# Performance work log

Measured on AMD Instinct MI355X. Metric: run time of the kernel, lower is better.

Reference implementation:

```python
import jax, jax.numpy as jnp
import numpy as np

N = 100000      # nodes
E = 1600000     # edges (avg degree 16)
IN, H, H4, OUT = 2, 128, 32, 64
B = 1000        # batch_size for final view


def setup_inputs() -> dict:
    key = jax.random.key(0)
    ks = jax.random.split(key, 16)
    w = lambda k, s: (jax.random.normal(k, s, jnp.float32) * (1.0 / np.sqrt(s[0])))
    return {
        "x": jax.random.normal(ks[0], (N, IN), jnp.float32),
        "edge_index": jax.random.randint(ks[1], (2, E), 0, N, dtype=jnp.int32),
        "batch_size": B,
        "W1": w(ks[2], (IN, H)),  "b1": jnp.zeros((H,), jnp.float32),
        "W2": w(ks[3], (H, H)),   "b2": jnp.zeros((H,), jnp.float32),
        "W3": w(ks[4], (H, H4)),  "b3": jnp.zeros((H4,), jnp.float32),
        "W4": w(ks[5], (H4, H4)), "b4": jnp.zeros((H4,), jnp.float32),
        "W5": w(ks[6], (H4, OUT)),"b5": jnp.zeros((OUT,), jnp.float32),
        "Wl": w(ks[7], (OUT, 1)), "bl": jnp.zeros((1,), jnp.float32),
    }


def gcn_conv(x, src, dst, W, b, n):
    # PyG GCNConv: add self-loops, symmetric degree normalization, scatter-add.
    h = x @ W  # [N, F]
    deg = jax.ops.segment_sum(jnp.ones(src.shape[0], h.dtype), dst,
                              num_segments=n) + 1.0  # +1 for self-loop
    dinv = jax.lax.rsqrt(deg)  # deg >= 1, no inf
    norm = dinv[src] * dinv[dst]  # [E]
    agg = jax.ops.segment_sum(h[src] * norm[:, None], dst, num_segments=n)
    agg = agg + h * (dinv * dinv)[:, None]  # self-loop contribution
    return agg + b


def reference(x, edge_index, batch_size, W1, b1, W2, b2, W3, b3, W4, b4, W5, b5, Wl, bl):
    x = x.reshape(-1, 2)
    n = x.shape[0]
    src, dst = edge_index[0], edge_index[1]
    for W, b in ((W1, b1), (W2, b2), (W3, b3), (W4, b4), (W5, b5)):
        x = jax.nn.relu(gcn_conv(x, src, dst, W, b, n))
    x = x @ Wl + bl  # [N, 1]
    return x.reshape(batch_size, -1)
```

## Files before the change

kernel.cpp:

```cpp
#include <hip/hip_runtime.h>
#include <math.h>


static inline int cdiv(int a, int b) { return (a + b - 1) / b; }

__global__ void zero_i32(int* __restrict__ p, int n) {
    int i = blockIdx.x * 256 + threadIdx.x;
    if (i < n) p[i] = 0;
}

__global__ void count_q(const int* __restrict__ src, const int* __restrict__ dst,
                        int* __restrict__ cntq, int E, int q1) {
    int e = blockIdx.x * 256 + threadIdx.x;
    if (e < E) {
        int s = src[e];
        int q = (s >= q1) + (s >= 2 * q1) + (s >= 3 * q1);
        atomicAdd(&cntq[dst[e] * 4 + q], 1);
    }
}

__global__ void scan1q(const int* __restrict__ cntq, int* __restrict__ off,
                       int* __restrict__ bsum, int n) {
    __shared__ int sm[256];
    int i = blockIdx.x * 256 + threadIdx.x;
    int v = 0;
    if (i < n) {
        int4 c = *reinterpret_cast<const int4*>(cntq + 4 * (size_t)i);
        v = c.x + c.y + c.z + c.w;
    }
    sm[threadIdx.x] = v;
    __syncthreads();
    for (int ofs = 1; ofs < 256; ofs <<= 1) {
        int t = (threadIdx.x >= (unsigned)ofs) ? sm[threadIdx.x - ofs] : 0;
        __syncthreads();
        sm[threadIdx.x] += t;
        __syncthreads();
    }
    if (i < n) off[i] = sm[threadIdx.x];
    if (threadIdx.x == 255) bsum[blockIdx.x] = sm[255];
}

__global__ void scan2(const int* __restrict__ bsum, int* __restrict__ bpre,
                      int nb, int* __restrict__ off, int N, int E) {
    __shared__ int sm[512];
    int t = threadIdx.x;
    sm[t] = (t < nb) ? bsum[t] : 0;
    __syncthreads();
    for (int ofs = 1; ofs < 512; ofs <<= 1) {
        int v = (t >= ofs) ? sm[t - ofs] : 0;
        __syncthreads();
        sm[t] += v;
        __syncthreads();
    }
    if (t < nb) bpre[t] = sm[t] - bsum[t];
    if (t == 0) off[N] = E;
}

__global__ void scan3_fused(const int* __restrict__ cntq, const int* __restrict__ bpre,
                            int* __restrict__ off, int* __restrict__ cursorq,
                            const float* __restrict__ x, float* __restrict__ dinv,
                            float* __restrict__ xs, int n) {
    int i = blockIdx.x * 256 + threadIdx.x;
    if (i < n) {
        int4 cq = *reinterpret_cast<const int4*>(cntq + 4 * (size_t)i);
        int c = cq.x + cq.y + cq.z + cq.w;
        int o = off[i] - c + bpre[blockIdx.x];
        off[i] = o;
        int4 cur;
        cur.x = o;
        cur.y = o + cq.x;
        cur.z = o + cq.x + cq.y;
        cur.w = o + cq.x + cq.y + cq.z;
        *reinterpret_cast<int4*>(cursorq + 4 * (size_t)i) = cur;
        float dv = 1.0f / sqrtf((float)c + 1.0f);
        dinv[i] = dv;
        float2 xv = *reinterpret_cast<const float2*>(x + 2 * (size_t)i);
        *reinterpret_cast<float2*>(xs + 2 * (size_t)i) = float2{dv * xv.x, dv * xv.y};
    }
}

__global__ __launch_bounds__(256) void fill_ranged(const int* __restrict__ src,
                                                   const int* __restrict__ dst,
                                                   int* __restrict__ cursorq,
                                                   int* __restrict__ csr,
                                                   int E, int N, int echunk, int q1) {
    int cls = blockIdx.x & 7;
    int chunk = blockIdx.x >> 3;
    int per = (N + 7) >> 3;
    int lo = cls * per;
    int hi = lo + per; if (hi > N) hi = N;
    int e0 = chunk * echunk;
    int e1 = e0 + echunk; if (e1 > E) e1 = E;
    for (int e = e0 + (int)threadIdx.x; e < e1; e += 256) {
        int d = dst[e];
        if (d >= lo && d < hi) {
            int s = src[e];
            int q = (s >= q1) + (s >= 2 * q1) + (s >= 3 * q1);
            int p = atomicAdd(&cursorq[d * 4 + q], 1);
            csr[p] = s;
        }
    }
}

__global__ __launch_bounds__(256) void agg2_kernel(const float* __restrict__ xs,
                                                   const int* __restrict__ off,
                                                   const int* __restrict__ csr,
                                                   const float* __restrict__ dinv,
                                                   float* __restrict__ out, int n) {
    int v = blockIdx.x * 256 + threadIdx.x;
    if (v >= n) return;
    float a0 = 0.f, a1 = 0.f;
    int e0 = off[v], e1 = off[v + 1];
    for (int e = e0; e < e1; e++) {
        int s = csr[e];
        float2 q = *reinterpret_cast<const float2*>(xs + 2 * (size_t)s);
        a0 += q.x;
        a1 += q.y;
    }
    float dv = dinv[v];
    float2 xv = *reinterpret_cast<const float2*>(xs + 2 * (size_t)v);
    *reinterpret_cast<float2*>(out + 2 * (size_t)v) =
        float2{dv * (a0 + xv.x), dv * (a1 + xv.y)};
}

template <bool BR, bool PS>
__global__ __launch_bounds__(256) void agg128x_kernel(const float* __restrict__ hc,
                                                      const int* __restrict__ off,
                                                      const int* __restrict__ csr,
                                                      const float* __restrict__ dinv,
                                                      const float* __restrict__ bias,
                                                      float* __restrict__ outc, int n) {
    int cls = blockIdx.x & 7;
    int chunk = cls >> 1;
    int half = cls & 1;
    int n2 = (n + 1) >> 1;
    int lo = half * n2;
    int hi = lo + n2; if (hi > n) hi = n;

    const float* __restrict__ h = hc + (size_t)chunk * n * 32;
    float* __restrict__ out = outc + (size_t)chunk * n * 32;

    int tid = threadIdx.x;
    int lane = tid & 63;
    int sl = lane & 7;
    int subbase = lane & ~7;
    int wave = tid >> 6;
    int v = lo + (blockIdx.x >> 3) * 32 + wave * 8 + (lane >> 3);
    if (v >= hi) return;

    int start = off[v];
    int end = off[v + 1];

    float4 acc = {0.f, 0.f, 0.f, 0.f};

    for (int base = start; base < end; base += 16) {
        int m = end - base;
        if (m > 16) m = 16;
        int idxA = (sl < m) ? csr[base + sl] : 0;
        int idxB = (8 + sl < m) ? csr[base + 8 + sl] : 0;
        if (m == 16) {
            float4 hb[16];
#pragma unroll
            for (int u = 0; u < 16; u++) {
                int s = __shfl((u < 8) ? idxA : idxB, subbase + (u & 7));
                hb[u] = *reinterpret_cast<const float4*>(h + (size_t)s * 32 + sl * 4);
            }
#pragma unroll
            for (int u = 0; u < 16; u++) {
                acc.x += hb[u].x; acc.y += hb[u].y; acc.z += hb[u].z; acc.w += hb[u].w;
            }
        } else {
            int ma = (m < 8) ? m : 8;
            int i = 0;
            for (; i + 4 <= ma; i += 4) {
                float4 hb[4];
#pragma unroll
                for (int u = 0; u < 4; u++) {
                    int s = __shfl(idxA, subbase + i + u);
                    hb[u] = *reinterpret_cast<const float4*>(h + (size_t)s * 32 + sl * 4);
                }
#pragma unroll
                for (int u = 0; u < 4; u++) {
                    acc.x += hb[u].x; acc.y += hb[u].y; acc.z += hb[u].z; acc.w += hb[u].w;
                }
            }
            if (i + 2 <= ma) {
                int s0 = __shfl(idxA, subbase + i);
                int s1 = __shfl(idxA, subbase + i + 1);
                float4 h0 = *reinterpret_cast<const float4*>(h + (size_t)s0 * 32 + sl * 4);
                float4 h1 = *reinterpret_cast<const float4*>(h + (size_t)s1 * 32 + sl * 4);
                acc.x += h0.x + h1.x; acc.y += h0.y + h1.y;
                acc.z += h0.z + h1.z; acc.w += h0.w + h1.w;
                i += 2;
            }
            if (i < ma) {
                int s0 = __shfl(idxA, subbase + i);
                float4 h0 = *reinterpret_cast<const float4*>(h + (size_t)s0 * 32 + sl * 4);
                acc.x += h0.x; acc.y += h0.y; acc.z += h0.z; acc.w += h0.w;
            }
            if (m > 8) {
                int mb = m - 8;
                int j = 0;
                for (; j + 4 <= mb; j += 4) {
                    float4 hb[4];
#pragma unroll
                    for (int u = 0; u < 4; u++) {
                        int s = __shfl(idxB, subbase + j + u);
                        hb[u] = *reinterpret_cast<const float4*>(h + (size_t)s * 32 + sl * 4);
                    }
#pragma unroll
                    for (int u = 0; u < 4; u++) {
                        acc.x += hb[u].x; acc.y += hb[u].y; acc.z += hb[u].z; acc.w += hb[u].w;
                    }
                }
                if (j + 2 <= mb) {
                    int s0 = __shfl(idxB, subbase + j);
                    int s1 = __shfl(idxB, subbase + j + 1);
                    float4 h0 = *reinterpret_cast<const float4*>(h + (size_t)s0 * 32 + sl * 4);
                    float4 h1 = *reinterpret_cast<const float4*>(h + (size_t)s1 * 32 + sl * 4);
                    acc.x += h0.x + h1.x; acc.y += h0.y + h1.y;
                    acc.z += h0.z + h1.z; acc.w += h0.w + h1.w;
                    j += 2;
                }
                if (j < mb) {
                    int s0 = __shfl(idxB, subbase + j);
                    float4 h0 = *reinterpret_cast<const float4*>(h + (size_t)s0 * 32 + sl * 4);
                    acc.x += h0.x; acc.y += h0.y; acc.z += h0.z; acc.w += h0.w;
                }
            }
        }
    }

    float dv = dinv[v];
    float4 hv = *reinterpret_cast<const float4*>(h + (size_t)v * 32 + sl * 4);
    float o0 = dv * (acc.x + hv.x);
    float o1 = dv * (acc.y + hv.y);
    float o2 = dv * (acc.z + hv.z);
    float o3 = dv * (acc.w + hv.w);
    if constexpr (BR) {
        float4 b = *reinterpret_cast<const float4*>(bias + chunk * 32 + sl * 4);
        o0 = fmaxf(o0 + b.x, 0.f);
        o1 = fmaxf(o1 + b.y, 0.f);
        o2 = fmaxf(o2 + b.z, 0.f);
        o3 = fmaxf(o3 + b.w, 0.f);
    }
    if constexpr (PS) {
        o0 *= dv; o1 *= dv; o2 *= dv; o3 *= dv;
    }
    *reinterpret_cast<float4*>(out + (size_t)v * 32 + sl * 4) = float4{o0, o1, o2, o3};
}

template <bool BR, bool PS>
__global__ __launch_bounds__(256) void agg32_kernel(const float* __restrict__ h,
                                                    const int* __restrict__ off,
                                                    const int* __restrict__ csr,
                                                    const float* __restrict__ dinv,
                                                    const float* __restrict__ bias,
                                                    float* __restrict__ out, int n) {
    int tid = threadIdx.x;
    int lane = tid & 63;
    int sl = lane & 7;
    int subbase = lane & ~7;
    int wave = tid >> 6;
    int v = blockIdx.x * 32 + wave * 8 + (lane >> 3);
    if (v >= n) return;

    int start = off[v];
    int end = off[v + 1];

    float4 acc = {0.f, 0.f, 0.f, 0.f};

    for (int base = start; base < end; base += 16) {
        int m = end - base;
        if (m > 16) m = 16;
        int idxA = (sl < m) ? csr[base + sl] : 0;
        int idxB = (8 + sl < m) ? csr[base + 8 + sl] : 0;
        if (m == 16) {
            float4 hb[16];
#pragma unroll
            for (int u = 0; u < 16; u++) {
                int s = __shfl((u < 8) ? idxA : idxB, subbase + (u & 7));
                hb[u] = *reinterpret_cast<const float4*>(h + (size_t)s * 32 + sl * 4);
            }
#pragma unroll
            for (int u = 0; u < 16; u++) {
                acc.x += hb[u].x; acc.y += hb[u].y; acc.z += hb[u].z; acc.w += hb[u].w;
            }
        } else {
            int ma = (m < 8) ? m : 8;
            int i = 0;
            for (; i + 4 <= ma; i += 4) {
                float4 hb[4];
#pragma unroll
                for (int u = 0; u < 4; u++) {
                    int s = __shfl(idxA, subbase + i + u);
                    hb[u] = *reinterpret_cast<const float4*>(h + (size_t)s * 32 + sl * 4);
                }
#pragma unroll
                for (int u = 0; u < 4; u++) {
                    acc.x += hb[u].x; acc.y += hb[u].y; acc.z += hb[u].z; acc.w += hb[u].w;
                }
            }
            if (i + 2 <= ma) {
                int s0 = __shfl(idxA, subbase + i);
                int s1 = __shfl(idxA, subbase + i + 1);
                float4 h0 = *reinterpret_cast<const float4*>(h + (size_t)s0 * 32 + sl * 4);
                float4 h1 = *reinterpret_cast<const float4*>(h + (size_t)s1 * 32 + sl * 4);
                acc.x += h0.x + h1.x; acc.y += h0.y + h1.y;
                acc.z += h0.z + h1.z; acc.w += h0.w + h1.w;
                i += 2;
            }
            if (i < ma) {
                int s0 = __shfl(idxA, subbase + i);
                float4 h0 = *reinterpret_cast<const float4*>(h + (size_t)s0 * 32 + sl * 4);
                acc.x += h0.x; acc.y += h0.y; acc.z += h0.z; acc.w += h0.w;
            }
            if (m > 8) {
                int mb = m - 8;
                int j = 0;
                for (; j + 4 <= mb; j += 4) {
                    float4 hb[4];
#pragma unroll
                    for (int u = 0; u < 4; u++) {
                        int s = __shfl(idxB, subbase + j + u);
                        hb[u] = *reinterpret_cast<const float4*>(h + (size_t)s * 32 + sl * 4);
                    }
#pragma unroll
                    for (int u = 0; u < 4; u++) {
                        acc.x += hb[u].x; acc.y += hb[u].y; acc.z += hb[u].z; acc.w += hb[u].w;
                    }
                }
                if (j + 2 <= mb) {
                    int s0 = __shfl(idxB, subbase + j);
                    int s1 = __shfl(idxB, subbase + j + 1);
                    float4 h0 = *reinterpret_cast<const float4*>(h + (size_t)s0 * 32 + sl * 4);
                    float4 h1 = *reinterpret_cast<const float4*>(h + (size_t)s1 * 32 + sl * 4);
                    acc.x += h0.x + h1.x; acc.y += h0.y + h1.y;
                    acc.z += h0.z + h1.z; acc.w += h0.w + h1.w;
                    j += 2;
                }
                if (j < mb) {
                    int s0 = __shfl(idxB, subbase + j);
                    float4 h0 = *reinterpret_cast<const float4*>(h + (size_t)s0 * 32 + sl * 4);
                    acc.x += h0.x; acc.y += h0.y; acc.z += h0.z; acc.w += h0.w;
                }
            }
        }
    }

    float dv = dinv[v];
    float4 hv = *reinterpret_cast<const float4*>(h + (size_t)v * 32 + sl * 4);
    float o0 = dv * (acc.x + hv.x);
    float o1 = dv * (acc.y + hv.y);
    float o2 = dv * (acc.z + hv.z);
    float o3 = dv * (acc.w + hv.w);
    if constexpr (BR) {
        float4 b = *reinterpret_cast<const float4*>(bias + sl * 4);
        o0 = fmaxf(o0 + b.x, 0.f);
        o1 = fmaxf(o1 + b.y, 0.f);
        o2 = fmaxf(o2 + b.z, 0.f);
        o3 = fmaxf(o3 + b.w, 0.f);
    }
    if constexpr (PS) {
        o0 *= dv; o1 *= dv; o2 *= dv; o3 *= dv;
    }
    *reinterpret_cast<float4*>(out + (size_t)v * 32 + sl * 4) = float4{o0, o1, o2, o3};
}

template <int K, int F, bool BR, bool PS, int CIN = 0, int COUT = 0>
__global__ __launch_bounds__(256, 4) void gemm_tiled(const float* __restrict__ x,
                                                     const float* __restrict__ W,
                                                     const float* __restrict__ bias,
                                                     const float* __restrict__ dinv,
                                                     float* __restrict__ h, int n) {
    constexpr int KC = 32;
    constexpr int KCP = 36;
    constexpr int ROWS = 64;
    constexpr int TPC = F / 4;
    constexpr int RT = 256 / TPC;
    constexpr int RPT = ROWS / RT;
    static_assert(K % KC == 0, "K must be a multiple of 32");

    __shared__ float Ws[KC * F];
    __shared__ float Xs[ROWS * KCP];

    const int tid = threadIdx.x;
    const int cb = (tid % TPC) * 4;
    const int tr = tid / TPC;
    const int row0 = blockIdx.x * ROWS;

    float acc[RPT][4];
#pragma unroll
    for (int r = 0; r < RPT; r++)
#pragma unroll
        for (int j = 0; j < 4; j++) acc[r][j] = 0.f;

#pragma unroll 1
    for (int k0 = 0; k0 < K; k0 += KC) {
        __syncthreads();
        {
            int r = tid >> 2;
            int kk = (tid & 3) * 8;
            int gr = row0 + r;
            float4 v0 = {0.f, 0.f, 0.f, 0.f}, v1 = {0.f, 0.f, 0.f, 0.f};
            if (gr < n) {
                if constexpr (CIN == 32) {
                    const float* xb = x + (size_t)(k0 >> 5) * n * 32 + (size_t)gr * 32 + kk;
                    v0 = *reinterpret_cast<const float4*>(xb);
                    v1 = *reinterpret_cast<const float4*>(xb + 4);
                } else {
                    v0 = *reinterpret_cast<const float4*>(x + (size_t)gr * K + k0 + kk);
                    v1 = *reinterpret_cast<const float4*>(x + (size_t)gr * K + k0 + kk + 4);
                }
            }
            *reinterpret_cast<float4*>(&Xs[r * KCP + kk]) = v0;
            *reinterpret_cast<float4*>(&Xs[r * KCP + kk + 4]) = v1;
        }
        for (int i = tid; i < KC * F / 4; i += 256) {
            *reinterpret_cast<float4*>(&Ws[i * 4]) =
                *reinterpret_cast<const float4*>(W + (size_t)k0 * F + i * 4);
        }
        __syncthreads();

#pragma unroll 4
        for (int kk4 = 0; kk4 < KC; kk4 += 4) {
            float4 xr[RPT];
#pragma unroll
            for (int r = 0; r < RPT; r++)
                xr[r] = *reinterpret_cast<const float4*>(&Xs[(tr * RPT + r) * KCP + kk4]);
#pragma unroll
            for (int j = 0; j < 4; j++) {
                float4 w = *reinterpret_cast<const float4*>(&Ws[(kk4 + j) * F + cb]);
#pragma unroll
                for (int r = 0; r < RPT; r++) {
                    float xv = (j == 0) ? xr[r].x : (j == 1) ? xr[r].y
                             : (j == 2) ? xr[r].z : xr[r].w;
                    acc[r][0] += xv * w.x;
                    acc[r][1] += xv * w.y;
                    acc[r][2] += xv * w.z;
                    acc[r][3] += xv * w.w;
                }
            }
        }
    }

    float4 b = float4{0.f, 0.f, 0.f, 0.f};
    if constexpr (BR) b = *reinterpret_cast<const float4*>(bias + cb);
#pragma unroll
    for (int r = 0; r < RPT; r++) {
        int row = row0 + tr * RPT + r;
        if (row < n) {
            float o0 = acc[r][0], o1 = acc[r][1], o2 = acc[r][2], o3 = acc[r][3];
            if constexpr (BR) {
                o0 = fmaxf(o0 + b.x, 0.f);
                o1 = fmaxf(o1 + b.y, 0.f);
                o2 = fmaxf(o2 + b.z, 0.f);
                o3 = fmaxf(o3 + b.w, 0.f);
            }
            if constexpr (PS) {
                float dv = dinv[row];
                o0 *= dv; o1 *= dv; o2 *= dv; o3 *= dv;
            }
            if constexpr (COUT == 32) {
                float* hb = h + (size_t)(cb >> 5) * n * 32 + (size_t)row * 32 + (cb & 31);
                *reinterpret_cast<float4*>(hb) = float4{o0, o1, o2, o3};
            } else {
                *reinterpret_cast<float4*>(&h[(size_t)row * F + cb]) = float4{o0, o1, o2, o3};
            }
        }
    }
}

__global__ __launch_bounds__(256, 4) void gemm_final(const float* __restrict__ x,
                                                     const float* __restrict__ W,
                                                     const float* __restrict__ bias,
                                                     const float* __restrict__ Wl,
                                                     const float* __restrict__ bl,
                                                     float* __restrict__ out, int n) {
    constexpr int K = 32, F = 64;
    constexpr int KC = 32;
    constexpr int KCP = 36;
    constexpr int ROWS = 64;
    constexpr int TPC = F / 4;
    constexpr int RT = 256 / TPC;
    constexpr int RPT = ROWS / RT;

    __shared__ float Ws[KC * F];
    __shared__ float Xs[ROWS * KCP];
    __shared__ float wl[F];

    const int tid = threadIdx.x;
    if (tid < F) wl[tid] = Wl[tid];
    const int cb = (tid % TPC) * 4;
    const int tr = tid / TPC;
    const int row0 = blockIdx.x * ROWS;

    float acc[RPT][4];
#pragma unroll
    for (int r = 0; r < RPT; r++)
#pragma unroll
        for (int j = 0; j < 4; j++) acc[r][j] = 0.f;

    {
        {
            int r = tid >> 2;
            int kk = (tid & 3) * 8;
            int gr = row0 + r;
            float4 v0 = {0.f, 0.f, 0.f, 0.f}, v1 = {0.f, 0.f, 0.f, 0.f};
            if (gr < n) {
                v0 = *reinterpret_cast<const float4*>(x + (size_t)gr * K + kk);
                v1 = *reinterpret_cast<const float4*>(x + (size_t)gr * K + kk + 4);
            }
            *reinterpret_cast<float4*>(&Xs[r * KCP + kk]) = v0;
            *reinterpret_cast<float4*>(&Xs[r * KCP + kk + 4]) = v1;
        }
        for (int i = tid; i < KC * F / 4; i += 256) {
            *reinterpret_cast<float4*>(&Ws[i * 4]) =
                *reinterpret_cast<const float4*>(W + i * 4);
        }
        __syncthreads();

#pragma unroll 4
        for (int kk4 = 0; kk4 < KC; kk4 += 4) {
            float4 xr[RPT];
#pragma unroll
            for (int r = 0; r < RPT; r++)
                xr[r] = *reinterpret_cast<const float4*>(&Xs[(tr * RPT + r) * KCP + kk4]);
#pragma unroll
            for (int j = 0; j < 4; j++) {
                float4 w = *reinterpret_cast<const float4*>(&Ws[(kk4 + j) * F + cb]);
#pragma unroll
                for (int r = 0; r < RPT; r++) {
                    float xv = (j == 0) ? xr[r].x : (j == 1) ? xr[r].y
                             : (j == 2) ? xr[r].z : xr[r].w;
                    acc[r][0] += xv * w.x;
                    acc[r][1] += xv * w.y;
                    acc[r][2] += xv * w.z;
                    acc[r][3] += xv * w.w;
                }
            }
        }
    }

    float4 b = *reinterpret_cast<const float4*>(bias + cb);
    float4 w = *reinterpret_cast<const float4*>(&wl[cb]);
    float blv = bl[0];
#pragma unroll
    for (int r = 0; r < RPT; r++) {
        int row = row0 + tr * RPT + r;
        float o0 = fmaxf(acc[r][0] + b.x, 0.f);
        float o1 = fmaxf(acc[r][1] + b.y, 0.f);
        float o2 = fmaxf(acc[r][2] + b.z, 0.f);
        float o3 = fmaxf(acc[r][3] + b.w, 0.f);
        float partial = o0 * w.x + o1 * w.y + o2 * w.z + o3 * w.w;
        partial += __shfl_xor(partial, 8, 16);
        partial += __shfl_xor(partial, 4, 16);
        partial += __shfl_xor(partial, 2, 16);
        partial += __shfl_xor(partial, 1, 16);
        if ((tid & 15) == 0 && row < n) out[row] = partial + blv;
    }
}

template <int K, int F, bool BR, bool PS>
__global__ __launch_bounds__(256, 4) void gemm_small(const float* __restrict__ x,
                                                     const float* __restrict__ W,
                                                     const float* __restrict__ bias,
                                                     const float* __restrict__ dinv,
                                                     float* __restrict__ h, int n) {
    constexpr int TPR = F / 4;
    constexpr int ROWS = 256 / TPR;
    __shared__ float Ws[K * F];
    for (int i = threadIdx.x; i < K * F; i += 256) Ws[i] = W[i];
    __syncthreads();

    int tid = threadIdx.x;
    int cb = (tid % TPR) * 4;
    int r = blockIdx.x * ROWS + tid / TPR;
    if (r >= n) return;

    const float* xr = x + (size_t)r * K;
    float a0 = 0.f, a1 = 0.f, a2 = 0.f, a3 = 0.f;
#pragma unroll
    for (int k = 0; k < K; k++) {
        float xv = xr[k];
        float4 w = *reinterpret_cast<const float4*>(&Ws[k * F + cb]);
        a0 += xv * w.x; a1 += xv * w.y; a2 += xv * w.z; a3 += xv * w.w;
    }
    if constexpr (BR) {
        float4 b = *reinterpret_cast<const float4*>(bias + cb);
        a0 = fmaxf(a0 + b.x, 0.f);
        a1 = fmaxf(a1 + b.y, 0.f);
        a2 = fmaxf(a2 + b.z, 0.f);
        a3 = fmaxf(a3 + b.w, 0.f);
    }
    if constexpr (PS) {
        float dv = dinv[r];
        a0 *= dv; a1 *= dv; a2 *= dv; a3 *= dv;
    }
    *reinterpret_cast<float4*>(&h[(size_t)r * F + cb]) = float4{a0, a1, a2, a3};
}

extern "C" void kernel_launch(void* const* d_in, const int* in_sizes, int n_in,
                              void* d_out, int out_size, void* d_ws, size_t ws_size,
                              hipStream_t stream) {
    const float* x = (const float*)d_in[0];
    const int* ei = (const int*)d_in[1];
    const float* W1 = (const float*)d_in[3];
    const float* b1 = (const float*)d_in[4];
    const float* W2 = (const float*)d_in[5];
    const float* b2 = (const float*)d_in[6];
    const float* W3 = (const float*)d_in[7];
    const float* b3 = (const float*)d_in[8];
    const float* W4 = (const float*)d_in[9];
    const float* b4 = (const float*)d_in[10];
    const float* W5 = (const float*)d_in[11];
    const float* b5 = (const float*)d_in[12];
    const float* Wl = (const float*)d_in[13];
    const float* bl = (const float*)d_in[14];

    const int N = in_sizes[0] / 2;
    const int E = in_sizes[1] / 2;
    const int* src = ei;
    const int* dst = ei + E;

    char* wp = (char*)d_ws;
    auto alloc = [&](size_t bytes) -> void* {
        void* p = wp;
        wp += ((bytes + 255) / 256) * 256;
        return p;
    };
    int* cntq = (int*)alloc((size_t)N * 4 * 4);
    int* off = (int*)alloc((size_t)(N + 1) * 4);
    int* cursorq = (int*)alloc((size_t)N * 4 * 4);
    int* bsum = (int*)alloc(512 * 4);
    int* bpre = (int*)alloc(512 * 4);
    int* csr = (int*)alloc((size_t)E * 4);
    float* dinv = (float*)alloc((size_t)N * 4);
    float* xs2 = (float*)alloc((size_t)N * 2 * 4);
    float* t2 = (float*)alloc((size_t)N * 2 * 4);
    float* bufA = (float*)alloc((size_t)N * 128 * 4);
    float* bufB = (float*)alloc((size_t)N * 128 * 4);

    const int gN = cdiv(N, 256);
    const int gE = cdiv(E, 256);
    const int nb = gN;
    const int gT = cdiv(N, 64);
    const int q1 = (N + 3) / 4;

    const int NCHUNK = 128;
    const int echunk = cdiv(E, NCHUNK);
    const int gR = 8 * NCHUNK;

    const int gX = 8 * cdiv((N + 1) / 2, 32);

    zero_i32<<<cdiv(4 * N, 256), 256, 0, stream>>>(cntq, 4 * N);
    count_q<<<gE, 256, 0, stream>>>(src, dst, cntq, E, q1);
    scan1q<<<nb, 256, 0, stream>>>(cntq, off, bsum, N);
    scan2<<<1, 512, 0, stream>>>(bsum, bpre, nb, off, N, E);
    scan3_fused<<<nb, 256, 0, stream>>>(cntq, bpre, off, cursorq, x, dinv, xs2, N);
    fill_ranged<<<gR, 256, 0, stream>>>(src, dst, cursorq, csr, E, N, echunk, q1);

    agg2_kernel<<<gN, 256, 0, stream>>>(xs2, off, csr, dinv, t2, N);
    gemm_small<2, 128, true, true><<<cdiv(N, 8), 256, 0, stream>>>(t2, W1, b1, dinv, bufA, N);
    gemm_tiled<128, 128, false, false, 0, 32><<<gT, 256, 0, stream>>>(bufA, W2, nullptr, nullptr, bufB, N);
    agg128x_kernel<true, true><<<gX, 256, 0, stream>>>(bufB, off, csr, dinv, b2, bufA, N);
    gemm_tiled<128, 32, false, false, 32, 0><<<gT, 256, 0, stream>>>(bufA, W3, nullptr, nullptr, bufB, N);
    agg32_kernel<true, true><<<cdiv(N, 32), 256, 0, stream>>>(bufB, off, csr, dinv, b3, bufA, N);
    gemm_tiled<32, 32, false, false, 0, 0><<<gT, 256, 0, stream>>>(bufA, W4, nullptr, nullptr, bufB, N);
    agg32_kernel<true, true><<<cdiv(N, 32), 256, 0, stream>>>(bufB, off, csr, dinv, b4, bufA, N);
    agg32_kernel<false, false><<<cdiv(N, 32), 256, 0, stream>>>(bufA, off, csr, dinv, nullptr, bufB, N);
    gemm_final<<<gT, 256, 0, stream>>>(bufB, W5, b5, Wl, bl, (float*)d_out, N);
}
```

Baseline: 526.2 us.

## Make 128-wide aggregation persistent with source-quarter phases and grid barriers

Replaces the per-node 128-feature aggregation with a persistent-style kernel where each block owns 13 node groups and walks edges in four source-range quarters, using the quartered cursor array. Blocks synchronise between quarters with a global atomic barrier, so the whole grid gathers from the same quarter of the feature table at once and that quarter can stay in cache. The barrier relies on all blocks being co-resident and has a bounded spin timeout, so correctness depends on occupancy. Splitting neighbours into four phases also shortens the unrolled inner chunks. A no-op index expression is added to a GEMM store.

```diff
diff --git a/kernel.cpp b/kernel.cpp
--- a/kernel.cpp
+++ b/kernel.cpp
@@ -123,13 +123,15 @@
         float2{dv * (a0 + xv.x), dv * (a1 + xv.y)};
 }
 
-template <bool BR, bool PS>
-__global__ __launch_bounds__(256) void agg128x_kernel(const float* __restrict__ hc,
-                                                      const int* __restrict__ off,
-                                                      const int* __restrict__ csr,
-                                                      const float* __restrict__ dinv,
-                                                      const float* __restrict__ bias,
-                                                      float* __restrict__ outc, int n) {
+template <bool BR, bool PS, int NG>
+__global__ __launch_bounds__(256, 4) void agg128xp2_kernel(const float* __restrict__ hc,
+                                                           const int* __restrict__ off,
+                                                           const int* __restrict__ cur4,
+                                                           const int* __restrict__ csr,
+                                                           const float* __restrict__ dinv,
+                                                           const float* __restrict__ bias,
+                                                           float* __restrict__ outc,
+                                                           int* __restrict__ bar, int n) {
     int cls = blockIdx.x & 7;
     int chunk = cls >> 1;
     int half = cls & 1;
@@ -144,110 +146,127 @@
     int lane = tid & 63;
     int sl = lane & 7;
     int subbase = lane & ~7;
-    int wave = tid >> 6;
-    int v = lo + (blockIdx.x >> 3) * 32 + wave * 8 + (lane >> 3);
-    if (v >= hi) return;
-
-    int start = off[v];
-    int end = off[v + 1];
-
-    float4 acc = {0.f, 0.f, 0.f, 0.f};
-
-    for (int base = start; base < end; base += 16) {
-        int m = end - base;
-        if (m > 16) m = 16;
-        int idxA = (sl < m) ? csr[base + sl] : 0;
-        int idxB = (8 + sl < m) ? csr[base + 8 + sl] : 0;
-        if (m == 16) {
-            float4 hb[16];
-#pragma unroll
-            for (int u = 0; u < 16; u++) {
-                int s = __shfl((u < 8) ? idxA : idxB, subbase + (u & 7));
-                hb[u] = *reinterpret_cast<const float4*>(h + (size_t)s * 32 + sl * 4);
-            }
-#pragma unroll
-            for (int u = 0; u < 16; u++) {
-                acc.x += hb[u].x; acc.y += hb[u].y; acc.z += hb[u].z; acc.w += hb[u].w;
-            }
-        } else {
-            int ma = (m < 8) ? m : 8;
-            int i = 0;
-            for (; i + 4 <= ma; i += 4) {
-                float4 hb[4];
-#pragma unroll
-                for (int u = 0; u < 4; u++) {
-                    int s = __shfl(idxA, subbase + i + u);
-                    hb[u] = *reinterpret_cast<const float4*>(h + (size_t)s * 32 + sl * 4);
-                }
-#pragma unroll
-                for (int u = 0; u < 4; u++) {
-                    acc.x += hb[u].x; acc.y += hb[u].y; acc.z += hb[u].z; acc.w += hb[u].w;
-                }
-            }
-            if (i + 2 <= ma) {
-                int s0 = __shfl(idxA, subbase + i);
-                int s1 = __shfl(idxA, subbase + i + 1);
-                float4 h0 = *reinterpret_cast<const float4*>(h + (size_t)s0 * 32 + sl * 4);
-                float4 h1 = *reinterpret_cast<const float4*>(h + (size_t)s1 * 32 + sl * 4);
-                acc.x += h0.x + h1.x; acc.y += h0.y + h1.y;
-                acc.z += h0.z + h1.z; acc.w += h0.w + h1.w;
-                i += 2;
-            }
-            if (i < ma) {
-                int s0 = __shfl(idxA, subbase + i);
-                float4 h0 = *reinterpret_cast<const float4*>(h + (size_t)s0 * 32 + sl * 4);
-                acc.x += h0.x; acc.y += h0.y; acc.z += h0.z; acc.w += h0.w;
-            }
-            if (m > 8) {
-                int mb = m - 8;
-                int j = 0;
-                for (; j + 4 <= mb; j += 4) {
+    int grpid = tid >> 3;
+    int nstart = lo + (blockIdx.x >> 3) * (NG * 32);
+    int nblocks = (int)gridDim.x;
+
+    float4 acc[NG];
+#pragma unroll
+    for (int g = 0; g < NG; g++) acc[g] = float4{0.f, 0.f, 0.f, 0.f};
+
+#pragma unroll 1
+    for (int q = 0; q < 4; q++) {
+        if (q > 0) {
+            if (tid == 0) {
+                atomicAdd(&bar[q], 1);
+                volatile int* vb = bar + q;
+                int it = 0;
+                while (*vb < nblocks && it < 20000) {
+                    __builtin_amdgcn_s_sleep(2);
+                    ++it;
+                }
+            }
+            __syncthreads();
+        }
+#pragma unroll
+        for (int g = 0; g < NG; g++) {
+            int v = nstart + g * 32 + grpid;
+            if (v >= hi) continue;
+            int s0 = (q == 0) ? off[v] : cur4[v * 4 + q - 1];
+            int s1 = cur4[v * 4 + q];
+            for (int base = s0; base < s1; base += 8) {
+                int m = s1 - base; if (m > 8) m = 8;
+                int idx = (sl < m) ? csr[base + sl] : 0;
+                int mA = (m < 4) ? m : 4;
+                if (mA == 4) {
                     float4 hb[4];
 #pragma unroll
                     for (int u = 0; u < 4; u++) {
-                        int s = __shfl(idxB, subbase + j + u);
+                        int s = __shfl(idx, subbase + u);
                         hb[u] = *reinterpret_cast<const float4*>(h + (size_t)s * 32 + sl * 4);
                     }
 #pragma unroll
                     for (int u = 0; u < 4; u++) {
-                        acc.x += hb[u].x; acc.y += hb[u].y; acc.z += hb[u].z; acc.w += hb[u].w;
+                        acc[g].x += hb[u].x; acc[g].y += hb[u].y;
+                        acc[g].z += hb[u].z; acc[g].w += hb[u].w;
                     }
-                }
-                if (j + 2 <= mb) {
-                    int s0 = __shfl(idxB, subbase + j);
-                    int s1 = __shfl(idxB, subbase + j + 1);
-                    float4 h0 = *reinterpret_cast<const float4*>(h + (size_t)s0 * 32 + sl * 4);
-                    float4 h1 = *reinterpret_cast<const float4*>(h + (size_t)s1 * 32 + sl * 4);
-                    acc.x += h0.x + h1.x; acc.y += h0.y + h1.y;
-                    acc.z += h0.z + h1.z; acc.w += h0.w + h1.w;
-                    j += 2;
-                }
-                if (j < mb) {
-                    int s0 = __shfl(idxB, subbase + j);
-                    float4 h0 = *reinterpret_cast<const float4*>(h + (size_t)s0 * 32 + sl * 4);
-                    acc.x += h0.x; acc.y += h0.y; acc.z += h0.z; acc.w += h0.w;
-                }
-            }
-        }
-    }
-
-    float dv = dinv[v];
-    float4 hv = *reinterpret_cast<const float4*>(h + (size_t)v * 32 + sl * 4);
-    float o0 = dv * (acc.x + hv.x);
-    float o1 = dv * (acc.y + hv.y);
-    float o2 = dv * (acc.z + hv.z);
-    float o3 = dv * (acc.w + hv.w);
-    if constexpr (BR) {
-        float4 b = *reinterpret_cast<const float4*>(bias + chunk * 32 + sl * 4);
-        o0 = fmaxf(o0 + b.x, 0.f);
-        o1 = fmaxf(o1 + b.y, 0.f);
-        o2 = fmaxf(o2 + b.z, 0.f);
-        o3 = fmaxf(o3 + b.w, 0.f);
-    }
-    if constexpr (PS) {
-        o0 *= dv; o1 *= dv; o2 *= dv; o3 *= dv;
-    }
-    *reinterpret_cast<float4*>(out + (size_t)v * 32 + sl * 4) = float4{o0, o1, o2, o3};
+                } else {
+                    int i = 0;
+                    if (i + 2 <= mA) {
+                        int sa = __shfl(idx, subbase + i);
+                        int sb = __shfl(idx, subbase + i + 1);
+                        float4 h0 = *reinterpret_cast<const float4*>(h + (size_t)sa * 32 + sl * 4);
+                        float4 h1 = *reinterpret_cast<const float4*>(h + (size_t)sb * 32 + sl * 4);
+                        acc[g].x += h0.x + h1.x; acc[g].y += h0.y + h1.y;
+                        acc[g].z += h0.z + h1.z; acc[g].w += h0.w + h1.w;
+                        i += 2;
+                    }
+                    if (i < mA) {
+                        int sa = __shfl(idx, subbase + i);
+                        float4 h0 = *reinterpret_cast<const float4*>(h + (size_t)sa * 32 + sl * 4);
+                        acc[g].x += h0.x; acc[g].y += h0.y;
+                        acc[g].z += h0.z; acc[g].w += h0.w;
+                    }
+                }
+                if (m > 4) {
+                    int mB = m - 4;
+                    if (mB == 4) {
+                        float4 hb[4];
+#pragma unroll
+                        for (int u = 0; u < 4; u++) {
+                            int s = __shfl(idx, subbase + 4 + u);
+                            hb[u] = *reinterpret_cast<const float4*>(h + (size_t)s * 32 + sl * 4);
+                        }
+#pragma unroll
+                        for (int u = 0; u < 4; u++) {
+                            acc[g].x += hb[u].x; acc[g].y += hb[u].y;
+                            acc[g].z += hb[u].z; acc[g].w += hb[u].w;
+                        }
+                    } else {
+                        int j = 0;
+                        if (j + 2 <= mB) {
+                            int sa = __shfl(idx, subbase + 4 + j);
+                            int sb = __shfl(idx, subbase + 4 + j + 1);
+                            float4 h0 = *reinterpret_cast<const float4*>(h + (size_t)sa * 32 + sl * 4);
+                            float4 h1 = *reinterpret_cast<const float4*>(h + (size_t)sb * 32 + sl * 4);
+                            acc[g].x += h0.x + h1.x; acc[g].y += h0.y + h1.y;
+                            acc[g].z += h0.z + h1.z; acc[g].w += h0.w + h1.w;
+                            j += 2;
+                        }
+                        if (j < mB) {
+                            int sa = __shfl(idx, subbase + 4 + j);
+                            float4 h0 = *reinterpret_cast<const float4*>(h + (size_t)sa * 32 + sl * 4);
+                            acc[g].x += h0.x; acc[g].y += h0.y;
+                            acc[g].z += h0.z; acc[g].w += h0.w;
+                        }
+                    }
+                }
+            }
+        }
+    }
+
+#pragma unroll
+    for (int g = 0; g < NG; g++) {
+        int v = nstart + g * 32 + grpid;
+        if (v >= hi) continue;
+        float dv = dinv[v];
+        float4 hv = *reinterpret_cast<const float4*>(h + (size_t)v * 32 + sl * 4);
+        float o0 = dv * (acc[g].x + hv.x);
+        float o1 = dv * (acc[g].y + hv.y);
+        float o2 = dv * (acc[g].z + hv.z);
+        float o3 = dv * (acc[g].w + hv.w);
+        if constexpr (BR) {
+            float4 b = *reinterpret_cast<const float4*>(bias + chunk * 32 + sl * 4);
+            o0 = fmaxf(o0 + b.x, 0.f);
+            o1 = fmaxf(o1 + b.y, 0.f);
+            o2 = fmaxf(o2 + b.z, 0.f);
+            o3 = fmaxf(o3 + b.w, 0.f);
+        }
+        if constexpr (PS) {
+            o0 *= dv; o1 *= dv; o2 *= dv; o3 *= dv;
+        }
+        *reinterpret_cast<float4*>(out + (size_t)v * 32 + sl * 4) = float4{o0, o1, o2, o3};
+    }
 }
 
 template <bool BR, bool PS>
@@ -597,7 +616,7 @@
         float dv = dinv[r];
         a0 *= dv; a1 *= dv; a2 *= dv; a3 *= dv;
     }
-    *reinterpret_cast<float4*>(&h[(size_t)r * F + cb]) = float4{a0, a1, a2, a3};
+    *reinterpret_cast<float4*>(&h[(size_t)r * K * 0 + (size_t)r * F + cb]) = float4{a0, a1, a2, a3};
 }
 
 extern "C" void kernel_launch(void* const* d_in, const int* in_sizes, int n_in,
@@ -634,6 +653,7 @@
     int* cursorq = (int*)alloc((size_t)N * 4 * 4);
     int* bsum = (int*)alloc(512 * 4);
     int* bpre = (int*)alloc(512 * 4);
+    int* bar = (int*)alloc(64 * 4);
     int* csr = (int*)alloc((size_t)E * 4);
     float* dinv = (float*)alloc((size_t)N * 4);
     float* xs2 = (float*)alloc((size_t)N * 2 * 4);
@@ -651,9 +671,12 @@
     const int echunk = cdiv(E, NCHUNK);
     const int gR = 8 * NCHUNK;
 
-    const int gX = 8 * cdiv((N + 1) / 2, 32);
+    constexpr int NG = 13;
+    const int BPC = cdiv((N + 1) / 2, NG * 32);
+    const int gP = 8 * BPC;
 
     zero_i32<<<cdiv(4 * N, 256), 256, 0, stream>>>(cntq, 4 * N);
+    zero_i32<<<1, 256, 0, stream>>>(bar, 64);
     count_q<<<gE, 256, 0, stream>>>(src, dst, cntq, E, q1);
     scan1q<<<nb, 256, 0, stream>>>(cntq, off, bsum, N);
     scan2<<<1, 512, 0, stream>>>(bsum, bpre, nb, off, N, E);
@@ -663,7 +686,7 @@
     agg2_kernel<<<gN, 256, 0, stream>>>(xs2, off, csr, dinv, t2, N);
     gemm_small<2, 128, true, true><<<cdiv(N, 8), 256, 0, stream>>>(t2, W1, b1, dinv, bufA, N);
     gemm_tiled<128, 128, false, false, 0, 32><<<gT, 256, 0, stream>>>(bufA, W2, nullptr, nullptr, bufB, N);
-    agg128x_kernel<true, true><<<gX, 256, 0, stream>>>(bufB, off, csr, dinv, b2, bufA, N);
+    agg128xp2_kernel<true, true, NG><<<gP, 256, 0, stream>>>(bufB, off, cursorq, csr, dinv, b2, bufA, bar, N);
     gemm_tiled<128, 32, false, false, 32, 0><<<gT, 256, 0, stream>>>(bufA, W3, nullptr, nullptr, bufB, N);
     agg32_kernel<true, true><<<cdiv(N, 32), 256, 0, stream>>>(bufB, off, csr, dinv, b3, bufA, N);
     gemm_tiled<32, 32, false, false, 0, 0><<<gT, 256, 0, stream>>>(bufA, W4, nullptr, nullptr, bufB, N);
```

Result: slower. 801.0 us (+52.2%).

## Fuse 32-wide GEMMs into neighbor aggregation epilogues for layers 3-5

Applied to the files above, without the earlier changes.

Moves the 32x32 W4 matmul into the layer-3 aggregation epilogue, computed with shuffles across the 8 lanes that own a node and W4 held in shared memory. Fuses the W5 matmul, bias, ReLU and final linear reduction into the last aggregation kernel. This removes two GEMM launches and their full N×32 intermediate write and read passes. In exchange each aggregation thread does extra shuffles and FMAs in its epilogue, and the common gather loop is moved into a shared device helper.

```diff
diff --git a/kernel.cpp b/kernel.cpp
--- a/kernel.cpp
+++ b/kernel.cpp
@@ -250,6 +250,91 @@
     *reinterpret_cast<float4*>(out + (size_t)v * 32 + sl * 4) = float4{o0, o1, o2, o3};
 }
 
+__device__ __forceinline__ float4 agg32_gather(const float* __restrict__ h,
+                                               const int* __restrict__ csr,
+                                               int start, int end,
+                                               int sl, int subbase) {
+    float4 acc = {0.f, 0.f, 0.f, 0.f};
+    for (int base = start; base < end; base += 16) {
+        int m = end - base;
+        if (m > 16) m = 16;
+        int idxA = (sl < m) ? csr[base + sl] : 0;
+        int idxB = (8 + sl < m) ? csr[base + 8 + sl] : 0;
+        if (m == 16) {
+            float4 hb[16];
+#pragma unroll
+            for (int u = 0; u < 16; u++) {
+                int s = __shfl((u < 8) ? idxA : idxB, subbase + (u & 7));
+                hb[u] = *reinterpret_cast<const float4*>(h + (size_t)s * 32 + sl * 4);
+            }
+#pragma unroll
+            for (int u = 0; u < 16; u++) {
+                acc.x += hb[u].x; acc.y += hb[u].y; acc.z += hb[u].z; acc.w += hb[u].w;
+            }
+        } else {
+            int ma = (m < 8) ? m : 8;
+            int i = 0;
+            for (; i + 4 <= ma; i += 4) {
+                float4 hb[4];
+#pragma unroll
+                for (int u = 0; u < 4; u++) {
+                    int s = __shfl(idxA, subbase + i + u);
+                    hb[u] = *reinterpret_cast<const float4*>(h + (size_t)s * 32 + sl * 4);
+                }
+#pragma unroll
+                for (int u = 0; u < 4; u++) {
+                    acc.x += hb[u].x; acc.y += hb[u].y; acc.z += hb[u].z; acc.w += hb[u].w;
+                }
+            }
+            if (i + 2 <= ma) {
+                int s0 = __shfl(idxA, subbase + i);
+                int s1 = __shfl(idxA, subbase + i + 1);
+                float4 h0 = *reinterpret_cast<const float4*>(h + (size_t)s0 * 32 + sl * 4);
+                float4 h1 = *reinterpret_cast<const float4*>(h + (size_t)s1 * 32 + sl * 4);
+                acc.x += h0.x + h1.x; acc.y += h0.y + h1.y;
+                acc.z += h0.z + h1.z; acc.w += h0.w + h1.w;
+                i += 2;
+            }
+            if (i < ma) {
+                int s0 = __shfl(idxA, subbase + i);
+                float4 h0 = *reinterpret_cast<const float4*>(h + (size_t)s0 * 32 + sl * 4);
+                acc.x += h0.x; acc.y += h0.y; acc.z += h0.z; acc.w += h0.w;
+            }
+            if (m > 8) {
+                int mb = m - 8;
+                int j = 0;
+                for (; j + 4 <= mb; j += 4) {
+                    float4 hb[4];
+#pragma unroll
+                    for (int u = 0; u < 4; u++) {
+                        int s = __shfl(idxB, subbase + j + u);
+                        hb[u] = *reinterpret_cast<const float4*>(h + (size_t)s * 32 + sl * 4);
+                    }
+#pragma unroll
+                    for (int u = 0; u < 4; u++) {
+                        acc.x += hb[u].x; acc.y += hb[u].y; acc.z += hb[u].z; acc.w += hb[u].w;
+                    }
+                }
+                if (j + 2 <= mb) {
+                    int s0 = __shfl(idxB, subbase + j);
+                    int s1 = __shfl(idxB, subbase + j + 1);
+                    float4 h0 = *reinterpret_cast<const float4*>(h + (size_t)s0 * 32 + sl * 4);
+                    float4 h1 = *reinterpret_cast<const float4*>(h + (size_t)s1 * 32 + sl * 4);
+                    acc.x += h0.x + h1.x; acc.y += h0.y + h1.y;
+                    acc.z += h0.z + h1.z; acc.w += h0.w + h1.w;
+                    j += 2;
+                }
+                if (j < mb) {
+                    int s0 = __shfl(idxB, subbase + j);
+                    float4 h0 = *reinterpret_cast<const float4*>(h + (size_t)s0 * 32 + sl * 4);
+                    acc.x += h0.x; acc.y += h0.y; acc.z += h0.z; acc.w += h0.w;
+                }
+            }
+        }
+    }
+    return acc;
+}
+
 template <bool BR, bool PS>
 __global__ __launch_bounds__(256) void agg32_kernel(const float* __restrict__ h,
                                                     const int* __restrict__ off,
@@ -265,88 +350,7 @@
     int v = blockIdx.x * 32 + wave * 8 + (lane >> 3);
     if (v >= n) return;
 
-    int start = off[v];
-    int end = off[v + 1];
-
-    float4 acc = {0.f, 0.f, 0.f, 0.f};
-
-    for (int base = start; base < end; base += 16) {
-        int m = end - base;
-        if (m > 16) m = 16;
-        int idxA = (sl < m) ? csr[base + sl] : 0;
-        int idxB = (8 + sl < m) ? csr[base + 8 + sl] : 0;
-        if (m == 16) {
-            float4 hb[16];
-#pragma unroll
-            for (int u = 0; u < 16; u++) {
-                int s = __shfl((u < 8) ? idxA : idxB, subbase + (u & 7));
-                hb[u] = *reinterpret_cast<const float4*>(h + (size_t)s * 32 + sl * 4);
-            }
-#pragma unroll
-            for (int u = 0; u < 16; u++) {
-                acc.x += hb[u].x; acc.y += hb[u].y; acc.z += hb[u].z; acc.w += hb[u].w;
-            }
-        } else {
-            int ma = (m < 8) ? m : 8;
-            int i = 0;
-            for (; i + 4 <= ma; i += 4) {
-                float4 hb[4];
-#pragma unroll
-                for (int u = 0; u < 4; u++) {
-                    int s = __shfl(idxA, subbase + i + u);
-                    hb[u] = *reinterpret_cast<const float4*>(h + (size_t)s * 32 + sl * 4);
-                }
-#pragma unroll
-                for (int u = 0; u < 4; u++) {
-                    acc.x += hb[u].x; acc.y += hb[u].y; acc.z += hb[u].z; acc.w += hb[u].w;
-                }
-            }
-            if (i + 2 <= ma) {
-                int s0 = __shfl(idxA, subbase + i);
-                int s1 = __shfl(idxA, subbase + i + 1);
-                float4 h0 = *reinterpret_cast<const float4*>(h + (size_t)s0 * 32 + sl * 4);
-                float4 h1 = *reinterpret_cast<const float4*>(h + (size_t)s1 * 32 + sl * 4);
-                acc.x += h0.x + h1.x; acc.y += h0.y + h1.y;
-                acc.z += h0.z + h1.z; acc.w += h0.w + h1.w;
-                i += 2;
-            }
-            if (i < ma) {
-                int s0 = __shfl(idxA, subbase + i);
-                float4 h0 = *reinterpret_cast<const float4*>(h + (size_t)s0 * 32 + sl * 4);
-                acc.x += h0.x; acc.y += h0.y; acc.z += h0.z; acc.w += h0.w;
-            }
-            if (m > 8) {
-                int mb = m - 8;
-                int j = 0;
-                for (; j + 4 <= mb; j += 4) {
-                    float4 hb[4];
-#pragma unroll
-                    for (int u = 0; u < 4; u++) {
-                        int s = __shfl(idxB, subbase + j + u);
-                        hb[u] = *reinterpret_cast<const float4*>(h + (size_t)s * 32 + sl * 4);
-                    }
-#pragma unroll
-                    for (int u = 0; u < 4; u++) {
-                        acc.x += hb[u].x; acc.y += hb[u].y; acc.z += hb[u].z; acc.w += hb[u].w;
-                    }
-                }
-                if (j + 2 <= mb) {
-                    int s0 = __shfl(idxB, subbase + j);
-                    int s1 = __shfl(idxB, subbase + j + 1);
-                    float4 h0 = *reinterpret_cast<const float4*>(h + (size_t)s0 * 32 + sl * 4);
-                    float4 h1 = *reinterpret_cast<const float4*>(h + (size_t)s1 * 32 + sl * 4);
-                    acc.x += h0.x + h1.x; acc.y += h0.y + h1.y;
-                    acc.z += h0.z + h1.z; acc.w += h0.w + h1.w;
-                    j += 2;
-                }
-                if (j < mb) {
-                    int s0 = __shfl(idxB, subbase + j);
-                    float4 h0 = *reinterpret_cast<const float4*>(h + (size_t)s0 * 32 + sl * 4);
-                    acc.x += h0.x; acc.y += h0.y; acc.z += h0.z; acc.w += h0.w;
-                }
-            }
-        }
-    }
+    float4 acc = agg32_gather(h, csr, off[v], off[v + 1], sl, subbase);
 
     float dv = dinv[v];
     float4 hv = *reinterpret_cast<const float4*>(h + (size_t)v * 32 + sl * 4);
@@ -365,6 +369,124 @@
         o0 *= dv; o1 *= dv; o2 *= dv; o3 *= dv;
     }
     *reinterpret_cast<float4*>(out + (size_t)v * 32 + sl * 4) = float4{o0, o1, o2, o3};
+}
+
+__global__ __launch_bounds__(256) void agg32mm_kernel(const float* __restrict__ h,
+                                                      const int* __restrict__ off,
+                                                      const int* __restrict__ csr,
+                                                      const float* __restrict__ dinv,
+                                                      const float* __restrict__ bias,
+                                                      const float* __restrict__ W,
+                                                      float* __restrict__ out, int n) {
+    __shared__ float Ws[32 * 32];
+    int tid = threadIdx.x;
+    *reinterpret_cast<float4*>(&Ws[tid * 4]) =
+        *reinterpret_cast<const float4*>(W + tid * 4);
+    __syncthreads();
+
+    int lane = tid & 63;
+    int sl = lane & 7;
+    int subbase = lane & ~7;
+    int wave = tid >> 6;
+    int v = blockIdx.x * 32 + wave * 8 + (lane >> 3);
+    if (v >= n) return;
+
+    float4 acc = agg32_gather(h, csr, off[v], off[v + 1], sl, subbase);
+
+    float dv = dinv[v];
+    float4 hv = *reinterpret_cast<const float4*>(h + (size_t)v * 32 + sl * 4);
+    float4 b = *reinterpret_cast<const float4*>(bias + sl * 4);
+    float o0 = fmaxf(dv * (acc.x + hv.x) + b.x, 0.f) * dv;
+    float o1 = fmaxf(dv * (acc.y + hv.y) + b.y, 0.f) * dv;
+    float o2 = fmaxf(dv * (acc.z + hv.z) + b.z, 0.f) * dv;
+    float o3 = fmaxf(dv * (acc.w + hv.w) + b.w, 0.f) * dv;
+
+    float y0 = 0.f, y1 = 0.f, y2 = 0.f, y3 = 0.f;
+#pragma unroll
+    for (int q = 0; q < 8; q++) {
+        float x0 = __shfl(o0, subbase + q);
+        float x1 = __shfl(o1, subbase + q);
+        float x2 = __shfl(o2, subbase + q);
+        float x3 = __shfl(o3, subbase + q);
+        float4 w0 = *reinterpret_cast<const float4*>(&Ws[(4 * q + 0) * 32 + sl * 4]);
+        float4 w1 = *reinterpret_cast<const float4*>(&Ws[(4 * q + 1) * 32 + sl * 4]);
+        float4 w2 = *reinterpret_cast<const float4*>(&Ws[(4 * q + 2) * 32 + sl * 4]);
+        float4 w3 = *reinterpret_cast<const float4*>(&Ws[(4 * q + 3) * 32 + sl * 4]);
+        y0 += x0 * w0.x + x1 * w1.x + x2 * w2.x + x3 * w3.x;
+        y1 += x0 * w0.y + x1 * w1.y + x2 * w2.y + x3 * w3.y;
+        y2 += x0 * w0.z + x1 * w1.z + x2 * w2.z + x3 * w3.z;
+        y3 += x0 * w0.w + x1 * w1.w + x2 * w2.w + x3 * w3.w;
+    }
+    *reinterpret_cast<float4*>(out + (size_t)v * 32 + sl * 4) = float4{y0, y1, y2, y3};
+}
+
+__global__ __launch_bounds__(256) void agg32fin_kernel(const float* __restrict__ h,
+                                                       const int* __restrict__ off,
+                                                       const int* __restrict__ csr,
+                                                       const float* __restrict__ dinv,
+                                                       const float* __restrict__ W5,
+                                                       const float* __restrict__ b5,
+                                                       const float* __restrict__ Wl,
+                                                       const float* __restrict__ bl,
+                                                       float* __restrict__ out, int n) {
+    __shared__ float W5s[32 * 64];
+    __shared__ float b5s[64];
+    __shared__ float wls[64];
+    int tid = threadIdx.x;
+    *reinterpret_cast<float4*>(&W5s[tid * 8]) =
+        *reinterpret_cast<const float4*>(W5 + tid * 8);
+    *reinterpret_cast<float4*>(&W5s[tid * 8 + 4]) =
+        *reinterpret_cast<const float4*>(W5 + tid * 8 + 4);
+    if (tid < 64) b5s[tid] = b5[tid];
+    else if (tid < 128) wls[tid - 64] = Wl[tid - 64];
+    __syncthreads();
+
+    int lane = tid & 63;
+    int sl = lane & 7;
+    int subbase = lane & ~7;
+    int wave = tid >> 6;
+    int v = blockIdx.x * 32 + wave * 8 + (lane >> 3);
+    if (v >= n) return;
+
+    float4 acc = agg32_gather(h, csr, off[v], off[v + 1], sl, subbase);
+
+    float dv = dinv[v];
+    float4 hv = *reinterpret_cast<const float4*>(h + (size_t)v * 32 + sl * 4);
+    float t0 = dv * (acc.x + hv.x);
+    float t1 = dv * (acc.y + hv.y);
+    float t2 = dv * (acc.z + hv.z);
+    float t3 = dv * (acc.w + hv.w);
+
+    float y0 = 0.f, y1 = 0.f, y2 = 0.f, y3 = 0.f;
+    float y4 = 0.f, y5 = 0.f, y6 = 0.f, y7 = 0.f;
+#pragma unroll
+    for (int q = 0; q < 8; q++) {
+        float x0 = __shfl(t0, subbase + q);
+        float x1 = __shfl(t1, subbase + q);
+        float x2 = __shfl(t2, subbase + q);
+        float x3 = __shfl(t3, subbase + q);
+#pragma unroll
+        for (int r = 0; r < 4; r++) {
+            float xv = (r == 0) ? x0 : (r == 1) ? x1 : (r == 2) ? x2 : x3;
+            const float* wr = &W5s[(4 * q + r) * 64 + sl * 8];
+            float4 wa = *reinterpret_cast<const float4*>(wr);
+            float4 wb = *reinterpret_cast<const float4*>(wr + 4);
+            y0 += xv * wa.x; y1 += xv * wa.y; y2 += xv * wa.z; y3 += xv * wa.w;
+            y4 += xv * wb.x; y5 += xv * wb.y; y6 += xv * wb.z; y7 += xv * wb.w;
+        }
+    }
+    float4 ba = *reinterpret_cast<const float4*>(&b5s[sl * 8]);
+    float4 bb = *reinterpret_cast<const float4*>(&b5s[sl * 8 + 4]);
+    float4 wa = *reinterpret_cast<const float4*>(&wls[sl * 8]);
+    float4 wb = *reinterpret_cast<const float4*>(&wls[sl * 8 + 4]);
+    float z = fmaxf(y0 + ba.x, 0.f) * wa.x + fmaxf(y1 + ba.y, 0.f) * wa.y +
+              fmaxf(y2 + ba.z, 0.f) * wa.z + fmaxf(y3 + ba.w, 0.f) * wa.w +
+              fmaxf(y4 + bb.x, 0.f) * wb.x + fmaxf(y5 + bb.y, 0.f) * wb.y +
+              fmaxf(y6 + bb.z, 0.f) * wb.z + fmaxf(y7 + bb.w, 0.f) * wb.w;
+    z += __shfl_xor(z, 4);
+    z += __shfl_xor(z, 2);
+    z += __shfl_xor(z, 1);
+    if (sl == 0) out[v] = z + bl[0];
 }
 
 template <int K, int F, bool BR, bool PS, int CIN = 0, int COUT = 0>
@@ -468,96 +590,6 @@
                 *reinterpret_cast<float4*>(&h[(size_t)row * F + cb]) = float4{o0, o1, o2, o3};
             }
         }
-    }
-}
-
-__global__ __launch_bounds__(256, 4) void gemm_final(const float* __restrict__ x,
-                                                     const float* __restrict__ W,
-                                                     const float* __restrict__ bias,
-                                                     const float* __restrict__ Wl,
-                                                     const float* __restrict__ bl,
-                                                     float* __restrict__ out, int n) {
-    constexpr int K = 32, F = 64;
-    constexpr int KC = 32;
-    constexpr int KCP = 36;
-    constexpr int ROWS = 64;
-    constexpr int TPC = F / 4;
-    constexpr int RT = 256 / TPC;
-    constexpr int RPT = ROWS / RT;
-
-    __shared__ float Ws[KC * F];
-    __shared__ float Xs[ROWS * KCP];
-    __shared__ float wl[F];
-
-    const int tid = threadIdx.x;
-    if (tid < F) wl[tid] = Wl[tid];
-    const int cb = (tid % TPC) * 4;
-    const int tr = tid / TPC;
-    const int row0 = blockIdx.x * ROWS;
-
-    float acc[RPT][4];
-#pragma unroll
-    for (int r = 0; r < RPT; r++)
-#pragma unroll
-        for (int j = 0; j < 4; j++) acc[r][j] = 0.f;
-
-    {
-        {
-            int r = tid >> 2;
-            int kk = (tid & 3) * 8;
-            int gr = row0 + r;
-            float4 v0 = {0.f, 0.f, 0.f, 0.f}, v1 = {0.f, 0.f, 0.f, 0.f};
-            if (gr < n) {
-                v0 = *reinterpret_cast<const float4*>(x + (size_t)gr * K + kk);
-                v1 = *reinterpret_cast<const float4*>(x + (size_t)gr * K + kk + 4);
-            }
-            *reinterpret_cast<float4*>(&Xs[r * KCP + kk]) = v0;
-            *reinterpret_cast<float4*>(&Xs[r * KCP + kk + 4]) = v1;
-        }
-        for (int i = tid; i < KC * F / 4; i += 256) {
-            *reinterpret_cast<float4*>(&Ws[i * 4]) =
-                *reinterpret_cast<const float4*>(W + i * 4);
-        }
-        __syncthreads();
-
-#pragma unroll 4
-        for (int kk4 = 0; kk4 < KC; kk4 += 4) {
-            float4 xr[RPT];
-#pragma unroll
-            for (int r = 0; r < RPT; r++)
-                xr[r] = *reinterpret_cast<const float4*>(&Xs[(tr * RPT + r) * KCP + kk4]);
-#pragma unroll
-            for (int j = 0; j < 4; j++) {
-                float4 w = *reinterpret_cast<const float4*>(&Ws[(kk4 + j) * F + cb]);
-#pragma unroll
-                for (int r = 0; r < RPT; r++) {
-                    float xv = (j == 0) ? xr[r].x : (j == 1) ? xr[r].y
-                             : (j == 2) ? xr[r].z : xr[r].w;
-                    acc[r][0] += xv * w.x;
-                    acc[r][1] += xv * w.y;
-                    acc[r][2] += xv * w.z;
-                    acc[r][3] += xv * w.w;
-                }
-            }
-        }
-    }
-
-    float4 b = *reinterpret_cast<const float4*>(bias + cb);
-    float4 w = *reinterpret_cast<const float4*>(&wl[cb]);
-    float blv = bl[0];
-#pragma unroll
-    for (int r = 0; r < RPT; r++) {
-        int row = row0 + tr * RPT + r;
-        float o0 = fmaxf(acc[r][0] + b.x, 0.f);
-        float o1 = fmaxf(acc[r][1] + b.y, 0.f);
-        float o2 = fmaxf(acc[r][2] + b.z, 0.f);
-        float o3 = fmaxf(acc[r][3] + b.w, 0.f);
-        float partial = o0 * w.x + o1 * w.y + o2 * w.z + o3 * w.w;
-        partial += __shfl_xor(partial, 8, 16);
-        partial += __shfl_xor(partial, 4, 16);
-        partial += __shfl_xor(partial, 2, 16);
-        partial += __shfl_xor(partial, 1, 16);
-        if ((tid & 15) == 0 && row < n) out[row] = partial + blv;
     }
 }
 
@@ -652,6 +684,7 @@
     const int gR = 8 * NCHUNK;
 
     const int gX = 8 * cdiv((N + 1) / 2, 32);
+    const int gA = cdiv(N, 32);
 
     zero_i32<<<cdiv(4 * N, 256), 256, 0, stream>>>(cntq, 4 * N);
     count_q<<<gE, 256, 0, stream>>>(src, dst, cntq, E, q1);
@@ -665,9 +698,7 @@
     gemm_tiled<128, 128, false, false, 0, 32><<<gT, 256, 0, stream>>>(bufA, W2, nullptr, nullptr, bufB, N);
     agg128x_kernel<true, true><<<gX, 256, 0, stream>>>(bufB, off, csr, dinv, b2, bufA, N);
     gemm_tiled<128, 32, false, false, 32, 0><<<gT, 256, 0, stream>>>(bufA, W3, nullptr, nullptr, bufB, N);
-    agg32_kernel<true, true><<<cdiv(N, 32), 256, 0, stream>>>(bufB, off, csr, dinv, b3, bufA, N);
-    gemm_tiled<32, 32, false, false, 0, 0><<<gT, 256, 0, stream>>>(bufA, W4, nullptr, nullptr, bufB, N);
-    agg32_kernel<true, true><<<cdiv(N, 32), 256, 0, stream>>>(bufB, off, csr, dinv, b4, bufA, N);
-    agg32_kernel<false, false><<<cdiv(N, 32), 256, 0, stream>>>(bufA, off, csr, dinv, nullptr, bufB, N);
-    gemm_final<<<gT, 256, 0, stream>>>(bufB, W5, b5, Wl, bl, (float*)d_out, N);
-}
+    agg32mm_kernel<<<gA, 256, 0, stream>>>(bufB, off, csr, dinv, b3, W4, bufA, N);
+    agg32_kernel<true, true><<<gA, 256, 0, stream>>>(bufA, off, csr, dinv, b4, bufB, N);
+    agg32fin_kernel<<<gA, 256, 0, stream>>>(bufB, off, csr, dinv, W5, b5, Wl, bl, (float*)d_out, N);
+}
```

After: 511.5 us. -2.8%, faster.
